# Optimization experiments

Measured on AMD Instinct MI355X. Metric: run time of the kernel, lower is better.

Reference implementation:

```python
import jax, jax.numpy as jnp
import numpy as np

NUM_BATCH = 8  # GroupNormalization(num_batch=num_groups) with num_groups=8
EPS = 1e-6


def setup_inputs() -> dict:
    key = jax.random.key(0)
    k1, k2, k3 = jax.random.split(key, 3)
    b, h, w, c = 32, 32, 32, 256
    x = jax.random.normal(k1, (b, h, w, c), dtype=jnp.float32)
    gamma = jnp.ones((c,), dtype=jnp.float32)
    beta = jnp.zeros((c,), dtype=jnp.float32)
    w_qkv = jax.random.normal(k2, (c, 3 * c), dtype=jnp.float32) * 0.02
    w_out = jax.random.normal(k3, (c, c), dtype=jnp.float32) * 0.02
    return {"x": x, "gamma": gamma, "beta": beta, "w_qkv": w_qkv, "w_out": w_out}


def reference(x, gamma, beta, w_qkv, w_out):
    b, h, w, c = x.shape
    # --- GroupNormalization (exact quirky semantics of the source) ---
    # num_groups = c // num_batch; reshape to [-1, num_groups, group_size]
    # -> per-(b,h,w)-pixel normalization over contiguous channel groups.
    ng = c // NUM_BATCH          # 32 groups
    gs = c // ng                 # 8 channels per group
    g = x.reshape(-1, ng, gs)
    mu = jnp.mean(g, axis=-1, keepdims=True)
    var = jnp.mean(jnp.square(g - mu), axis=-1, keepdims=True)
    xn = ((g - mu) / jnp.sqrt(var + EPS)).reshape(x.shape)
    xn = gamma * xn + beta
    # --- 1x1 conv to qkv (bias-free) ---
    qkv = jnp.einsum('bhwc,cd->bhwd', xn, w_qkv)  # [b,h,w,3c]
    q, k, v = jnp.split(qkv, 3, axis=-1)
    # self_attention=True branch: tie q=k=v to their mean
    t = (v + q + k) / 3.0
    q = k = v = t
    # --- exact reshapes from the source (raw reshapes, not transposes) ---
    q = jnp.transpose(q, (0, 3, 1, 2)).reshape(b, h * w, c)  # [b,hw,c]
    k = k.reshape(b, c, h * w)                               # [b,c,hw]
    v = jnp.transpose(v, (0, 3, 1, 2)).reshape(b, h * w, c)  # [b,hw,c]
    scores = jnp.matmul(q, k) * (c ** -0.5)                  # [b,hw,hw]
    attn = jax.nn.softmax(scores, axis=-1)
    # NOTE: source passes transpose_a=float (truthy) -> attention is transposed
    out = jnp.matmul(jnp.swapaxes(attn, 1, 2), v)            # [b,hw,c]
    out = out.reshape(b, h, w, c)
    return jnp.einsum('bhwc,cd->bhwd', out, w_out) + x
```

## Files before the change

kernel.cpp:

```cpp
#include <hip/hip_runtime.h>

typedef unsigned short u16;
typedef unsigned char u8;
typedef long long i64;
typedef __bf16 bf16x8 __attribute__((ext_vector_type(8)));
typedef float f32x4 __attribute__((ext_vector_type(4)));
typedef u16 u16x8 __attribute__((ext_vector_type(8)));

#define GLD16(g, l) __builtin_amdgcn_global_load_lds( \
    (const __attribute__((address_space(1))) void*)(g), \
    (__attribute__((address_space(3))) void*)(l), 16, 0, 0)
#define VMW(N) asm volatile("s_waitcnt vmcnt(" #N ")" ::: "memory")
#define SCHB __builtin_amdgcn_sched_barrier(0)
#define SBAR __builtin_amdgcn_s_barrier()

__device__ __forceinline__ float bf2f(u16 u) {
  return __uint_as_float(((unsigned)u) << 16);
}
__device__ __forceinline__ u16 f2bf(float f) {
  unsigned u = __float_as_uint(f);
  return (u16)((u + 0x7fffu + ((u >> 16) & 1u)) >> 16);
}
__device__ __forceinline__ u8 f8e_sw(float v) {
  unsigned u = __float_as_uint(v);
  unsigned s = (u >> 24) & 0x80u;
  u &= 0x7fffffffu;
  if (u < 0x3c000000u) return (u8)s;
  int b = (int)((u + 0x7FFFFu + ((u >> 20) & 1u)) >> 20) - 960;
  b = b < 8 ? 8 : (b > 126 ? 126 : b);
  return (u8)(b | s);
}
__device__ __forceinline__ float f8d_sw(u8 b) {
  if (!(b & 0x7f)) return 0.0f;
  float v = __uint_as_float((((unsigned)(b & 0x7fu)) << 20) + 0x3C000000u);
  return (b & 0x80u) ? -v : v;
}
__device__ __forceinline__ unsigned pk4(float a, float b, float c, float d) {
#if __has_builtin(__builtin_amdgcn_cvt_pk_fp8_f32)
  int r = __builtin_amdgcn_cvt_pk_fp8_f32(a, b, 0, false);
  r = __builtin_amdgcn_cvt_pk_fp8_f32(c, d, r, true);
  return (unsigned)r;
#else
  return (unsigned)f8e_sw(a) | ((unsigned)f8e_sw(b) << 8) |
         ((unsigned)f8e_sw(c) << 16) | ((unsigned)f8e_sw(d) << 24);
#endif
}
__device__ __forceinline__ float f8df(u8 b) {
#if __has_builtin(__builtin_amdgcn_cvt_f32_fp8)
  return __builtin_amdgcn_cvt_f32_fp8((int)b, 0);
#else
  return f8d_sw(b);
#endif
}
__device__ __forceinline__ int sig(int r) { return (r ^ (r >> 3)) & 7; }
__device__ __forceinline__ int wkey(int r) { return (r ^ (r >> 2)) & 3; }

__global__ void combine_w(const float* __restrict__ wqkv, const float* __restrict__ wout,
                          u16* __restrict__ wtT, u16* __restrict__ woutT) {
  int c = blockIdx.x, d = threadIdx.x;
  float t = (wqkv[c * 768 + d] + wqkv[c * 768 + 256 + d] + wqkv[c * 768 + 512 + d]) * (1.0f / 3.0f);
  wtT[d * 256 + c] = f2bf(t);
  woutT[d * 256 + c] = f2bf(wout[c * 256 + d]);
}

__global__ __launch_bounds__(512) void gnT(
    const float* __restrict__ x, const float* __restrict__ gamma,
    const float* __restrict__ beta, const u16* __restrict__ wtT,
    u8* __restrict__ Q8, u8* __restrict__ Kt8) {
  __shared__ u16 lA[2][64 * 64];
  __shared__ u16 lB[2][256 * 64];
  const int m0 = blockIdx.x * 64;
  const int z = m0 >> 10;
  const int t = threadIdx.x, lane = t & 63;
  const int w = t >> 6, wr = w >> 2, wc = w & 3;
  f32x4 acc[2][4] = {};

#define GNT_STAGE(B, K0)                                                        \
  {                                                                             \
    _Pragma("unroll") for (int ch = 0; ch < 4; ch++) {                          \
      int flat = ch * 512 + t, row = flat >> 3, slot = flat & 7;                \
      GLD16(wtT + (size_t)row * 256 + (K0) + (slot ^ sig(row)) * 8,             \
            lB[B] + flat * 8);                                                  \
    }                                                                           \
    int row = t >> 3, grp = t & 7;                                              \
    const float* xp = x + (size_t)(m0 + row) * 256 + (K0) + grp * 8;            \
    float4 a = *(const float4*)xp, b = *(const float4*)(xp + 4);                \
    float mu = (a.x + a.y + a.z + a.w + b.x + b.y + b.z + b.w) * 0.125f;        \
    float d0 = a.x - mu, d1 = a.y - mu, d2 = a.z - mu, d3 = a.w - mu;           \
    float d4 = b.x - mu, d5 = b.y - mu, d6 = b.z - mu, d7 = b.w - mu;           \
    float var = (d0 * d0 + d1 * d1 + d2 * d2 + d3 * d3 +                        \
                 d4 * d4 + d5 * d5 + d6 * d6 + d7 * d7) * 0.125f;               \
    float rs = rsqrtf(var + 1e-6f);                                             \
    const float4 g0 = *(const float4*)(gamma + (K0) + grp * 8);                 \
    const float4 g1 = *(const float4*)(gamma + (K0) + grp * 8 + 4);             \
    const float4 e0 = *(const float4*)(beta + (K0) + grp * 8);                  \
    const float4 e1 = *(const float4*)(beta + (K0) + grp * 8 + 4);              \
    u16x8 o;                                                                    \
    o[0] = f2bf(g0.x * (d0 * rs) + e0.x); o[1] = f2bf(g0.y * (d1 * rs) + e0.y); \
    o[2] = f2bf(g0.z * (d2 * rs) + e0.z); o[3] = f2bf(g0.w * (d3 * rs) + e0.w); \
    o[4] = f2bf(g1.x * (d4 * rs) + e1.x); o[5] = f2bf(g1.y * (d5 * rs) + e1.y); \
    o[6] = f2bf(g1.z * (d6 * rs) + e1.z); o[7] = f2bf(g1.w * (d7 * rs) + e1.w); \
    *(u16x8*)(lA[B] + row * 64 + (grp ^ sig(row)) * 8) = o;                     \
  }

  GNT_STAGE(0, 0);
  __syncthreads();
  for (int it = 0; it < 4; it++) {
    if (it < 3) { GNT_STAGE((it + 1) & 1, (it + 1) * 64); }
    const u16* la = lA[it & 1];
    const u16* lb = lB[it & 1];
#pragma unroll
    for (int kk = 0; kk < 2; kk++) {
      bf16x8 af[2], bfr[4];
#pragma unroll
      for (int mi = 0; mi < 2; mi++) {
        int m = wr * 32 + mi * 16 + (lane & 15);
        af[mi] = *(const bf16x8*)(la + m * 64 + ((kk * 32 + (lane >> 4) * 8) ^ (sig(m) << 3)));
      }
#pragma unroll
      for (int ni = 0; ni < 4; ni++) {
        int n = wc * 64 + ni * 16 + (lane & 15);
        bfr[ni] = *(const bf16x8*)(lb + n * 64 + ((kk * 32 + (lane >> 4) * 8) ^ (sig(n) << 3)));
      }
#pragma unroll
      for (int mi = 0; mi < 2; mi++)
#pragma unroll
        for (int ni = 0; ni < 4; ni++)
          acc[mi][ni] = __builtin_amdgcn_mfma_f32_16x16x32_bf16(af[mi], bfr[ni], acc[mi][ni], 0, 0, 0);
    }
    __syncthreads();
  }

  const int rb = m0 + wr * 32 + ((lane >> 4) << 2);
  const int cb = wc * 64 + (lane & 15);
  u8* kt = (u8*)lB[0];
  u8* qtile = (u8*)lB[1];
#pragma unroll
  for (int mi = 0; mi < 2; mi++)
#pragma unroll
    for (int ni = 0; ni < 4; ni++) {
      int P0 = rb + mi * 16, c = cb + ni * 16;
      int pl = P0 - m0;
      unsigned pk = pk4(acc[mi][ni][0], acc[mi][ni][1], acc[mi][ni][2], acc[mi][ni][3]);
#pragma unroll
      for (int j = 0; j < 4; j++)
        kt[(j * 256 + c) * 16 + (pl >> 2)] = (u8)(pk >> (8 * j));
      *(unsigned*)(qtile + c * 80 + pl) = pk;
    }
  __syncthreads();
  const int ckb = (m0 & 1023) >> 2;
  u8* Kz = Kt8 + (size_t)z * 262144;
  u8* Qz = Q8 + (size_t)z * 262144;
#pragma unroll
  for (int r2 = 0; r2 < 2; r2++) {
    int r = t * 2 + r2;
    uint4 v = *(const uint4*)(kt + r * 16);
    *(uint4*)(Kz + (size_t)r * 256 + ckb) = v;
  }
#pragma unroll
  for (int ph = 0; ph < 2; ph++) {
    int idx = ph * 512 + t, c = idx >> 2, q = idx & 3;
    uint4 v = *(const uint4*)(qtile + c * 80 + q * 16);
    *(uint4*)(Qz + (size_t)c * 1024 + (m0 & 1023) + q * 16) = v;
  }
#undef GNT_STAGE
}

__global__ __launch_bounds__(256) void gemm_s8(
    const u8* __restrict__ Q8, const u8* __restrict__ Kt8,
    u8* __restrict__ Et, float* __restrict__ partials) {
  __shared__ u8 lA[2][128 * 128];
  __shared__ u8 lB[2][128 * 128];
  const int z = blockIdx.x;
  const int mb = blockIdx.y & 7, pb = blockIdx.y >> 3;
  const u8* Az = Q8 + (size_t)z * 262144;
  const u8* Bz = Kt8 + (size_t)z * 262144;
  u8* Ez = Et + (size_t)z * 1048576;
  const int m0 = mb * 128, n0 = pb * 128;
  const int t = threadIdx.x, lane = t & 63;
  const int wr = (t >> 6) >> 1, wc = (t >> 6) & 1;
  f32x4 acc[4][4] = {};

#define S8_STAGE(B, K0)                                                       \
  {                                                                           \
    _Pragma("unroll") for (int ch = 0; ch < 4; ch++) {                        \
      int flat = ch * 256 + t, row = flat >> 3, slot = flat & 7;              \
      GLD16(Az + (size_t)(m0 + row) * 256 + (K0) + (slot ^ sig(row)) * 16,    \
            lA[B] + flat * 16);                                               \
    }                                                                         \
    _Pragma("unroll") for (int ch = 0; ch < 4; ch++) {                        \
      int flat = ch * 256 + t, row = flat >> 3, slot = flat & 7;              \
      GLD16(Bz + (size_t)(n0 + row) * 256 + (K0) + (slot ^ sig(row)) * 16,    \
            lB[B] + flat * 16);                                               \
    }                                                                         \
  }
#define S8_COMP(LA, LB)                                                       \
  _Pragma("unroll") for (int kk = 0; kk < 4; kk++) {                          \
    i64 af[4], bfv[4];                                                        \
    int koff = kk * 32 + (lane >> 4) * 8;                                     \
    _Pragma("unroll") for (int mi = 0; mi < 4; mi++) {                        \
      int m = wr * 64 + mi * 16 + (lane & 15);                                \
      af[mi] = *(const i64*)((LA) + m * 128 + (koff ^ (sig(m) << 4)));        \
    }                                                                         \
    _Pragma("unroll") for (int ni = 0; ni < 4; ni++) {                        \
      int n = wc * 64 + ni * 16 + (lane & 15);                                \
      bfv[ni] = *(const i64*)((LB) + n * 128 + (koff ^ (sig(n) << 4)));       \
    }                                                                         \
    _Pragma("unroll") for (int mi = 0; mi < 4; mi++)                          \
      _Pragma("unroll") for (int ni = 0; ni < 4; ni++)                        \
        acc[mi][ni] = __builtin_amdgcn_mfma_f32_16x16x32_fp8_fp8(             \
            af[mi], bfv[ni], acc[mi][ni], 0, 0, 0);                           \
  }

  S8_STAGE(0, 0);
  S8_STAGE(1, 128);
  VMW(8); SCHB; SBAR; SCHB;
  __builtin_amdgcn_s_setprio(1);
  S8_COMP(lA[0], lB[0]);
  __builtin_amdgcn_s_setprio(0);
  VMW(0); SCHB; SBAR; SCHB;
  __builtin_amdgcn_s_setprio(1);
  S8_COMP(lA[1], lB[1]);
  __builtin_amdgcn_s_setprio(0);
  __syncthreads();
#undef S8_STAGE
#undef S8_COMP

  u8* ldsC = lA[0];
  const int rbl = wr * 64 + ((lane >> 4) << 2);
  const int cbl = wc * 64 + (lane & 15);
  const float SCL = 0.0625f * 1.44269504089f;
  float ps[4][4] = {};
#pragma unroll
  for (int mi = 0; mi < 4; mi++)
#pragma unroll
    for (int ni = 0; ni < 4; ni++) {
      int pl = cbl + ni * 16, ib = rbl + mi * 16;
      float e0 = exp2f(acc[mi][ni][0] * SCL);
      float e1 = exp2f(acc[mi][ni][1] * SCL);
      float e2 = exp2f(acc[mi][ni][2] * SCL);
      float e3 = exp2f(acc[mi][ni][3] * SCL);
      ps[mi][0] += e0; ps[mi][1] += e1; ps[mi][2] += e2; ps[mi][3] += e3;
      *(unsigned*)(ldsC + pl * 128 + (ib ^ ((pl & 7) << 4))) = pk4(e0, e1, e2, e3);
    }
#pragma unroll
  for (int mi = 0; mi < 4; mi++)
#pragma unroll
    for (int j = 0; j < 4; j++) {
      float v = ps[mi][j];
      v += __shfl_xor(v, 1); v += __shfl_xor(v, 2);
      v += __shfl_xor(v, 4); v += __shfl_xor(v, 8);
      if ((lane & 15) == 0)
        partials[(size_t)(z * 1024 + m0 + rbl + mi * 16 + j) * 16 + pb * 2 + wc] = v;
    }
  __syncthreads();
#pragma unroll
  for (int ph = 0; ph < 4; ph++) {
    int pl = ph * 32 + (t >> 3), ich = (t & 7) * 16;
    uint4 v = *(const uint4*)(ldsC + pl * 128 + (ich ^ ((pl & 7) << 4)));
    *(uint4*)(Ez + (size_t)(n0 + pl) * 1024 + m0 + ich) = v;
  }
}

__global__ __launch_bounds__(256) void qt8(
    const u8* __restrict__ Q8, const float* __restrict__ partials, u8* __restrict__ Qt) {
  __shared__ u8 tile[64][260];
  __shared__ float rv[64];
  const int z = blockIdx.y, i0 = blockIdx.x * 64;
  const u8* src = Q8 + (size_t)z * 262144;
  u8* dst = Qt + (size_t)z * 262144;
  const int t = threadIdx.x;
#pragma unroll
  for (int q = 0; q < 4; q++) {
    uint4 v = *(const uint4*)(src + (size_t)(i0 + (t >> 2)) * 256 + (t & 3) * 64 + q * 16);
    *(uint4*)(&tile[t >> 2][(t & 3) * 64 + q * 16]) = v;
  }
  if (t < 64) {
    const float4* p = (const float4*)(partials + (size_t)(z * 1024 + i0 + t) * 16);
    float4 a = p[0], b = p[1], c = p[2], d = p[3];
    float s = ((a.x + a.y) + (a.z + a.w)) + ((b.x + b.y) + (b.z + b.w)) +
              ((c.x + c.y) + (c.z + c.w)) + ((d.x + d.y) + (d.z + d.w));
    rv[t] = 1024.0f / s;
  }
  __syncthreads();
#pragma unroll
  for (int q = 0; q < 4; q++) {
    unsigned wd[4];
#pragma unroll
    for (int d = 0; d < 4; d++) {
      float f[4];
#pragma unroll
      for (int e = 0; e < 4; e++) {
        int i = q * 16 + d * 4 + e;
        f[e] = f8df(tile[i][t]) * rv[i];
      }
      wd[d] = pk4(f[0], f[1], f[2], f[3]);
    }
    uint4 v = {wd[0], wd[1], wd[2], wd[3]};
    *(uint4*)(dst + (size_t)t * 1024 + i0 + q * 16) = v;
  }
}

__global__ __launch_bounds__(512, 4) void gemm_of(
    const u8* __restrict__ Et, const u8* __restrict__ Qt,
    const u16* __restrict__ woutT, const float* __restrict__ x,
    float* __restrict__ C) {
  __shared__ char smem[81920];
  const int z = blockIdx.x;
  const int m0 = blockIdx.y * 64;
  const u8* Az = Et + (size_t)z * 1048576;
  const u8* Bz = Qt + (size_t)z * 262144;
  const int t = threadIdx.x, lane = t & 63;
  const int w = t >> 6, wr = w >> 2, wc = w & 3;
  f32x4 acc[2][4] = {};

#define O8_STAGE(B, K0)                                                       \
  {                                                                           \
    u8* la_ = (u8*)smem + (B) * 8192;                                         \
    u8* lb_ = (u8*)smem + 16384 + (B) * 32768;                                \
    {                                                                         \
      int row = t >> 3, slot = t & 7;                                         \
      GLD16(Az + (size_t)(m0 + row) * 1024 + (K0) + (slot ^ sig(row)) * 16,   \
            la_ + t * 16);                                                    \
    }                                                                         \
    _Pragma("unroll") for (int ch = 0; ch < 4; ch++) {                        \
      int flat = ch * 512 + t, row = flat >> 3, slot = flat & 7;              \
      GLD16(Bz + (size_t)row * 1024 + (K0) + (slot ^ sig(row)) * 16,          \
            lb_ + flat * 16);                                                 \
    }                                                                         \
  }

  O8_STAGE(0, 0);
  for (int it = 0; it < 8; it++) {
    if (it < 7) {
      O8_STAGE((it + 1) & 1, (it + 1) * 128);
      VMW(5);
    } else {
      VMW(0);
    }
    SCHB; SBAR; SCHB;
    const u8* la = (const u8*)smem + (it & 1) * 8192;
    const u8* lb = (const u8*)smem + 16384 + (it & 1) * 32768;
    __builtin_amdgcn_s_setprio(1);
#pragma unroll
    for (int kk = 0; kk < 4; kk++) {
      i64 af[2], bfv[4];
      int koff = kk * 32 + (lane >> 4) * 8;
#pragma unroll
      for (int mi = 0; mi < 2; mi++) {
        int m = wr * 32 + mi * 16 + (lane & 15);
        af[mi] = *(const i64*)(la + m * 128 + (koff ^ (sig(m) << 4)));
      }
#pragma unroll
      for (int ni = 0; ni < 4; ni++) {
        int n = wc * 64 + ni * 16 + (lane & 15);
        bfv[ni] = *(const i64*)(lb + n * 128 + (koff ^ (sig(n) << 4)));
      }
#pragma unroll
      for (int mi = 0; mi < 2; mi++)
#pragma unroll
        for (int ni = 0; ni < 4; ni++)
          acc[mi][ni] = __builtin_amdgcn_mfma_f32_16x16x32_fp8_fp8(af[mi], bfv[ni], acc[mi][ni], 0, 0, 0);
    }
    __builtin_amdgcn_s_setprio(0);
    SBAR;
  }
#undef O8_STAGE

#define W_STAGE(B, K0)                                                        \
  {                                                                           \
    u8* wb_ = (u8*)smem + 32768 + (B) * 16384;                                \
    _Pragma("unroll") for (int ch = 0; ch < 2; ch++) {                        \
      int flat = ch * 512 + t, row = flat >> 2, slot = flat & 3;              \
      GLD16(woutT + (size_t)row * 256 + (K0) + (slot ^ wkey(row)) * 8,        \
            wb_ + flat * 16);                                                 \
    }                                                                         \
  }
  W_STAGE(0, 0);
  {
#pragma unroll
    for (int mi = 0; mi < 2; mi++)
#pragma unroll
      for (int ni = 0; ni < 4; ni++)
#pragma unroll
        for (int j = 0; j < 4; j++) {
          int pl = wr * 32 + mi * 16 + ((lane >> 4) << 2) + j;
          int c = wc * 64 + ni * 16 + (lane & 15);
          int byteoff = (pl * 512 + c * 2) ^ ((pl & 7) << 4);
          *(u16*)(smem + byteoff) = f2bf(acc[mi][ni][j] * (1.0f / 1024.0f));
        }
  }
  asm volatile("s_waitcnt lgkmcnt(0)" ::: "memory");
  SCHB; SBAR; SCHB;

  f32x4 acc2[2][4] = {};
  for (int it2 = 0; it2 < 8; it2++) {
    if (it2 < 7) {
      W_STAGE((it2 + 1) & 1, (it2 + 1) * 32);
      VMW(2);
    } else {
      VMW(0);
    }
    SCHB; SBAR; SCHB;
    const u8* wb = (const u8*)smem + 32768 + (it2 & 1) * 16384;
    __builtin_amdgcn_s_setprio(1);
    {
      bf16x8 af2[2], bfr[4];
#pragma unroll
      for (int mi = 0; mi < 2; mi++) {
        int m = wr * 32 + mi * 16 + (lane & 15);
        int kg = (it2 * 32 + (lane >> 4) * 8) * 2;
        af2[mi] = *(const bf16x8*)(smem + ((m * 512 + kg) ^ ((m & 7) << 4)));
      }
#pragma unroll
      for (int ni = 0; ni < 4; ni++) {
        int n = wc * 64 + ni * 16 + (lane & 15);
        int s = lane >> 4;
        bfr[ni] = *(const bf16x8*)(wb + n * 64 + (s ^ wkey(n)) * 16);
      }
#pragma unroll
      for (int mi = 0; mi < 2; mi++)
#pragma unroll
        for (int ni = 0; ni < 4; ni++)
          acc2[mi][ni] = __builtin_amdgcn_mfma_f32_16x16x32_bf16(af2[mi], bfr[ni], acc2[mi][ni], 0, 0, 0);
    }
    __builtin_amdgcn_s_setprio(0);
    SBAR;
  }
#undef W_STAGE

  {
#pragma unroll
    for (int mi = 0; mi < 2; mi++)
#pragma unroll
      for (int ni = 0; ni < 4; ni++)
#pragma unroll
        for (int j = 0; j < 4; j++) {
          int pl = wr * 32 + mi * 16 + ((lane >> 4) << 2) + j;
          int c = wc * 64 + ni * 16 + (lane & 15);
          *(float*)(smem + ((pl * 1024 + c * 4) ^ ((pl & 7) << 4))) = acc2[mi][ni][j];
        }
    __syncthreads();
    const size_t base = ((size_t)z * 1024 + m0) * 256;
#pragma unroll
    for (int pi = 0; pi < 8; pi++) {
      int f4 = pi * 512 + t;
      int row = f4 >> 6, ch = f4 & 63;
      f32x4 a = *(const f32x4*)(smem + row * 1024 + ((ch * 16) ^ ((row & 7) << 4)));
      const float4 xv = *(const float4*)(x + base + (size_t)f4 * 4);
      float4 o;
      o.x = a[0] + xv.x; o.y = a[1] + xv.y; o.z = a[2] + xv.z; o.w = a[3] + xv.w;
      *(float4*)(C + base + (size_t)f4 * 4) = o;
    }
  }
}

extern "C" void kernel_launch(void* const* d_in, const int* in_sizes, int n_in,
                              void* d_out, int out_size, void* d_ws, size_t ws_size,
                              hipStream_t stream) {
  (void)in_sizes; (void)n_in; (void)out_size; (void)ws_size;
  const float* x = (const float*)d_in[0];
  const float* gamma = (const float*)d_in[1];
  const float* beta = (const float*)d_in[2];
  const float* wqkv = (const float*)d_in[3];
  const float* wout = (const float*)d_in[4];
  float* outp = (float*)d_out;

  char* ws = (char*)d_ws;
  const size_t MB = 1024 * 1024;
  u16* wtT = (u16*)(ws + 0);
  u16* woutT = (u16*)(ws + (128 << 10));
  float* partials = (float*)(ws + (512 << 10));
  u8* Q8 = (u8*)(ws + 3 * MB);
  u8* Kt8 = (u8*)(ws + 12 * MB);
  u8* Qt = (u8*)(ws + 21 * MB);
  u8* Et = (u8*)(ws + 30 * MB);

  combine_w<<<256, 256, 0, stream>>>(wqkv, wout, wtT, woutT);
  gnT<<<512, 512, 0, stream>>>(x, gamma, beta, wtT, Q8, Kt8);
  gemm_s8<<<dim3(32, 64), 256, 0, stream>>>(Q8, Kt8, Et, partials);
  qt8<<<dim3(16, 32), 256, 0, stream>>>(Q8, partials, Qt);
  gemm_of<<<dim3(32, 16), 512, 0, stream>>>(Et, Qt, woutT, x, outp);
}
```

Measured before the change: 90.13 us.

## Reassociate output projection: fold W_out into V before attention GEMM

Instead of computing attn^T·V and then multiplying by W_out in bf16 inside the final kernel, a new gemm_g kernel precomputes G = (V scaled by softmax normalizers)·W_out in fp8 per batch, replacing the qt8 transpose kernel. The final kernel then does a single fp8 GEMM of E^T with G plus the residual, removing the second bf16 GEMM stage and its weight streaming. W_out is stored as scaled fp8 instead of bf16, adding quantization error on the projected values.

New measurement: 85.81 us. -4.8%, faster.

```diff
diff --git a/kernel.cpp b/kernel.cpp
--- a/kernel.cpp
+++ b/kernel.cpp
@@ -29,11 +29,6 @@
   int b = (int)((u + 0x7FFFFu + ((u >> 20) & 1u)) >> 20) - 960;
   b = b < 8 ? 8 : (b > 126 ? 126 : b);
   return (u8)(b | s);
-}
-__device__ __forceinline__ float f8d_sw(u8 b) {
-  if (!(b & 0x7f)) return 0.0f;
-  float v = __uint_as_float((((unsigned)(b & 0x7fu)) << 20) + 0x3C000000u);
-  return (b & 0x80u) ? -v : v;
 }
 __device__ __forceinline__ unsigned pk4(float a, float b, float c, float d) {
 #if __has_builtin(__builtin_amdgcn_cvt_pk_fp8_f32)
@@ -45,22 +40,21 @@
          ((unsigned)f8e_sw(c) << 16) | ((unsigned)f8e_sw(d) << 24);
 #endif
 }
-__device__ __forceinline__ float f8df(u8 b) {
-#if __has_builtin(__builtin_amdgcn_cvt_f32_fp8)
-  return __builtin_amdgcn_cvt_f32_fp8((int)b, 0);
+__device__ __forceinline__ u8 f8e1(float v) {
+#if __has_builtin(__builtin_amdgcn_cvt_pk_fp8_f32)
+  return (u8)(__builtin_amdgcn_cvt_pk_fp8_f32(v, v, 0, false) & 0xff);
 #else
-  return f8d_sw(b);
+  return f8e_sw(v);
 #endif
 }
 __device__ __forceinline__ int sig(int r) { return (r ^ (r >> 3)) & 7; }
-__device__ __forceinline__ int wkey(int r) { return (r ^ (r >> 2)) & 3; }
 
 __global__ void combine_w(const float* __restrict__ wqkv, const float* __restrict__ wout,
-                          u16* __restrict__ wtT, u16* __restrict__ woutT) {
+                          u16* __restrict__ wtT, u8* __restrict__ wout8) {
   int c = blockIdx.x, d = threadIdx.x;
   float t = (wqkv[c * 768 + d] + wqkv[c * 768 + 256 + d] + wqkv[c * 768 + 512 + d]) * (1.0f / 3.0f);
   wtT[d * 256 + c] = f2bf(t);
-  woutT[d * 256 + c] = f2bf(wout[c * 256 + d]);
+  wout8[d * 256 + c] = f8e1(64.0f * wout[c * 256 + d]);
 }
 
 __global__ __launch_bounds__(512) void gnT(
@@ -262,59 +256,93 @@
   }
 }
 
-__global__ __launch_bounds__(256) void qt8(
-    const u8* __restrict__ Q8, const float* __restrict__ partials, u8* __restrict__ Qt) {
-  __shared__ u8 tile[64][260];
-  __shared__ float rv[64];
-  const int z = blockIdx.y, i0 = blockIdx.x * 64;
-  const u8* src = Q8 + (size_t)z * 262144;
-  u8* dst = Qt + (size_t)z * 262144;
-  const int t = threadIdx.x;
-#pragma unroll
-  for (int q = 0; q < 4; q++) {
-    uint4 v = *(const uint4*)(src + (size_t)(i0 + (t >> 2)) * 256 + (t & 3) * 64 + q * 16);
-    *(uint4*)(&tile[t >> 2][(t & 3) * 64 + q * 16]) = v;
-  }
-  if (t < 64) {
+__global__ __launch_bounds__(512) void gemm_g(
+    const u8* __restrict__ wout8, const u8* __restrict__ Q8,
+    const float* __restrict__ partials, u8* __restrict__ Gt) {
+  __shared__ u8 lA[256 * 256];
+  __shared__ u8 lB[128 * 256];
+  __shared__ float rv[128];
+  const int z = blockIdx.x;
+  const int i0 = blockIdx.y * 128;
+  const u8* Bz = Q8 + (size_t)z * 262144;
+  u8* Gz = Gt + (size_t)z * 262144;
+  const int t = threadIdx.x, lane = t & 63;
+  const int w = t >> 6, wr = w >> 2, wc = w & 3;
+#pragma unroll
+  for (int ch = 0; ch < 8; ch++) {
+    int flat = ch * 512 + t, row = flat >> 4, slot = flat & 15;
+    GLD16(wout8 + (size_t)row * 256 + (slot ^ sig(row)) * 16, lA + flat * 16);
+  }
+#pragma unroll
+  for (int ch = 0; ch < 4; ch++) {
+    int flat = ch * 512 + t, row = flat >> 4, slot = flat & 15;
+    GLD16(Bz + (size_t)(i0 + row) * 256 + (slot ^ sig(row)) * 16, lB + flat * 16);
+  }
+  if (t < 128) {
     const float4* p = (const float4*)(partials + (size_t)(z * 1024 + i0 + t) * 16);
     float4 a = p[0], b = p[1], c = p[2], d = p[3];
     float s = ((a.x + a.y) + (a.z + a.w)) + ((b.x + b.y) + (b.z + b.w)) +
               ((c.x + c.y) + (c.z + c.w)) + ((d.x + d.y) + (d.z + d.w));
-    rv[t] = 1024.0f / s;
-  }
-  __syncthreads();
-#pragma unroll
-  for (int q = 0; q < 4; q++) {
-    unsigned wd[4];
-#pragma unroll
-    for (int d = 0; d < 4; d++) {
-      float f[4];
-#pragma unroll
-      for (int e = 0; e < 4; e++) {
-        int i = q * 16 + d * 4 + e;
-        f[e] = f8df(tile[i][t]) * rv[i];
+    rv[t] = 128.0f / s;
+  }
+  __syncthreads();
+  f32x4 acc[8][2] = {};
+#pragma unroll
+  for (int kk = 0; kk < 8; kk++) {
+    i64 af[8], bfv[2];
+    int koff = kk * 32 + (lane >> 4) * 8;
+#pragma unroll
+    for (int mi = 0; mi < 8; mi++) {
+      int m = wr * 128 + mi * 16 + (lane & 15);
+      af[mi] = *(const i64*)(lA + m * 256 + (koff ^ (sig(m) << 4)));
+    }
+#pragma unroll
+    for (int ni = 0; ni < 2; ni++) {
+      int n = wc * 32 + ni * 16 + (lane & 15);
+      bfv[ni] = *(const i64*)(lB + n * 256 + (koff ^ (sig(n) << 4)));
+    }
+#pragma unroll
+    for (int mi = 0; mi < 8; mi++)
+#pragma unroll
+      for (int ni = 0; ni < 2; ni++)
+        acc[mi][ni] = __builtin_amdgcn_mfma_f32_16x16x32_fp8_fp8(af[mi], bfv[ni], acc[mi][ni], 0, 0, 0);
+  }
+  __syncthreads();
+  u8* ldsG = lB;
+#pragma unroll
+  for (int mi = 0; mi < 8; mi++)
+#pragma unroll
+    for (int ni = 0; ni < 2; ni++) {
+      int i = wc * 32 + ni * 16 + (lane & 15);
+      float r = rv[i];
+#pragma unroll
+      for (int j = 0; j < 4; j++) {
+        int d = wr * 128 + mi * 16 + ((lane >> 4) << 2) + j;
+        ldsG[d * 128 + (i ^ ((d & 7) << 4))] = f8e1(acc[mi][ni][j] * r);
       }
-      wd[d] = pk4(f[0], f[1], f[2], f[3]);
-    }
-    uint4 v = {wd[0], wd[1], wd[2], wd[3]};
-    *(uint4*)(dst + (size_t)t * 1024 + i0 + q * 16) = v;
-  }
-}
-
-__global__ __launch_bounds__(512, 4) void gemm_of(
-    const u8* __restrict__ Et, const u8* __restrict__ Qt,
-    const u16* __restrict__ woutT, const float* __restrict__ x,
-    float* __restrict__ C) {
+    }
+  __syncthreads();
+#pragma unroll
+  for (int ch = 0; ch < 4; ch++) {
+    int flat = ch * 512 + t, d = flat >> 3, q = flat & 7;
+    uint4 v = *(const uint4*)(ldsG + d * 128 + ((q * 16) ^ ((d & 7) << 4)));
+    *(uint4*)(Gz + (size_t)d * 1024 + i0 + q * 16) = v;
+  }
+}
+
+__global__ __launch_bounds__(512, 4) void gemm_fin(
+    const u8* __restrict__ Et, const u8* __restrict__ Gt,
+    const float* __restrict__ x, float* __restrict__ C) {
   __shared__ char smem[81920];
   const int z = blockIdx.x;
   const int m0 = blockIdx.y * 64;
   const u8* Az = Et + (size_t)z * 1048576;
-  const u8* Bz = Qt + (size_t)z * 262144;
+  const u8* Bz = Gt + (size_t)z * 262144;
   const int t = threadIdx.x, lane = t & 63;
   const int w = t >> 6, wr = w >> 2, wc = w & 3;
   f32x4 acc[2][4] = {};
 
-#define O8_STAGE(B, K0)                                                       \
+#define FIN_STAGE(B, K0)                                                      \
   {                                                                           \
     u8* la_ = (u8*)smem + (B) * 8192;                                         \
     u8* lb_ = (u8*)smem + 16384 + (B) * 32768;                                \
@@ -330,10 +358,10 @@
     }                                                                         \
   }
 
-  O8_STAGE(0, 0);
+  FIN_STAGE(0, 0);
   for (int it = 0; it < 8; it++) {
     if (it < 7) {
-      O8_STAGE((it + 1) & 1, (it + 1) * 128);
+      FIN_STAGE((it + 1) & 1, (it + 1) * 128);
       VMW(5);
     } else {
       VMW(0);
@@ -365,18 +393,8 @@
     __builtin_amdgcn_s_setprio(0);
     SBAR;
   }
-#undef O8_STAGE
-
-#define W_STAGE(B, K0)                                                        \
-  {                                                                           \
-    u8* wb_ = (u8*)smem + 32768 + (B) * 16384;                                \
-    _Pragma("unroll") for (int ch = 0; ch < 2; ch++) {                        \
-      int flat = ch * 512 + t, row = flat >> 2, slot = flat & 3;              \
-      GLD16(woutT + (size_t)row * 256 + (K0) + (slot ^ wkey(row)) * 8,        \
-            wb_ + flat * 16);                                                 \
-    }                                                                         \
-  }
-  W_STAGE(0, 0);
+#undef FIN_STAGE
+
   {
 #pragma unroll
     for (int mi = 0; mi < 2; mi++)
@@ -386,59 +404,8 @@
         for (int j = 0; j < 4; j++) {
           int pl = wr * 32 + mi * 16 + ((lane >> 4) << 2) + j;
           int c = wc * 64 + ni * 16 + (lane & 15);
-          int byteoff = (pl * 512 + c * 2) ^ ((pl & 7) << 4);
-          *(u16*)(smem + byteoff) = f2bf(acc[mi][ni][j] * (1.0f / 1024.0f));
-        }
-  }
-  asm volatile("s_waitcnt lgkmcnt(0)" ::: "memory");
-  SCHB; SBAR; SCHB;
-
-  f32x4 acc2[2][4] = {};
-  for (int it2 = 0; it2 < 8; it2++) {
-    if (it2 < 7) {
-      W_STAGE((it2 + 1) & 1, (it2 + 1) * 32);
-      VMW(2);
-    } else {
-      VMW(0);
-    }
-    SCHB; SBAR; SCHB;
-    const u8* wb = (const u8*)smem + 32768 + (it2 & 1) * 16384;
-    __builtin_amdgcn_s_setprio(1);
-    {
-      bf16x8 af2[2], bfr[4];
-#pragma unroll
-      for (int mi = 0; mi < 2; mi++) {
-        int m = wr * 32 + mi * 16 + (lane & 15);
-        int kg = (it2 * 32 + (lane >> 4) * 8) * 2;
-        af2[mi] = *(const bf16x8*)(smem + ((m * 512 + kg) ^ ((m & 7) << 4)));
-      }
-#pragma unroll
-      for (int ni = 0; ni < 4; ni++) {
-        int n = wc * 64 + ni * 16 + (lane & 15);
-        int s = lane >> 4;
-        bfr[ni] = *(const bf16x8*)(wb + n * 64 + (s ^ wkey(n)) * 16);
-      }
-#pragma unroll
-      for (int mi = 0; mi < 2; mi++)
-#pragma unroll
-        for (int ni = 0; ni < 4; ni++)
-          acc2[mi][ni] = __builtin_amdgcn_mfma_f32_16x16x32_bf16(af2[mi], bfr[ni], acc2[mi][ni], 0, 0, 0);
-    }
-    __builtin_amdgcn_s_setprio(0);
-    SBAR;
-  }
-#undef W_STAGE
-
-  {
-#pragma unroll
-    for (int mi = 0; mi < 2; mi++)
-#pragma unroll
-      for (int ni = 0; ni < 4; ni++)
-#pragma unroll
-        for (int j = 0; j < 4; j++) {
-          int pl = wr * 32 + mi * 16 + ((lane >> 4) << 2) + j;
-          int c = wc * 64 + ni * 16 + (lane & 15);
-          *(float*)(smem + ((pl * 1024 + c * 4) ^ ((pl & 7) << 4))) = acc2[mi][ni][j];
+          *(float*)(smem + ((pl * 1024 + c * 4) ^ ((pl & 7) << 4))) =
+              acc[mi][ni][j] * (1.0f / 8192.0f);
         }
     __syncthreads();
     const size_t base = ((size_t)z * 1024 + m0) * 256;
@@ -469,16 +436,16 @@
   char* ws = (char*)d_ws;
   const size_t MB = 1024 * 1024;
   u16* wtT = (u16*)(ws + 0);
-  u16* woutT = (u16*)(ws + (128 << 10));
+  u8* wout8 = (u8*)(ws + (128 << 10));
   float* partials = (float*)(ws + (512 << 10));
   u8* Q8 = (u8*)(ws + 3 * MB);
   u8* Kt8 = (u8*)(ws + 12 * MB);
-  u8* Qt = (u8*)(ws + 21 * MB);
+  u8* Gt = (u8*)(ws + 21 * MB);
   u8* Et = (u8*)(ws + 30 * MB);
 
-  combine_w<<<256, 256, 0, stream>>>(wqkv, wout, wtT, woutT);
+  combine_w<<<256, 256, 0, stream>>>(wqkv, wout, wtT, wout8);
   gnT<<<512, 512, 0, stream>>>(x, gamma, beta, wtT, Q8, Kt8);
   gemm_s8<<<dim3(32, 64), 256, 0, stream>>>(Q8, Kt8, Et, partials);
-  qt8<<<dim3(16, 32), 256, 0, stream>>>(Q8, partials, Qt);
-  gemm_of<<<dim3(32, 16), 512, 0, stream>>>(Et, Qt, woutT, x, outp);
-}
+  gemm_g<<<dim3(32, 8), 512, 0, stream>>>(wout8, Q8, partials, Gt);
+  gemm_fin<<<dim3(32, 16), 512, 0, stream>>>(Et, Gt, x, outp);
+}
```
